# Kernel tuning notes

Hardware: AMD Instinct MI355X
Metric: run time of the kernel (lower is better)

The kernel has to match this reference:

```python
import jax, jax.numpy as jnp
import numpy as np

ANCHORS = np.array([[30.0, 61.0], [62.0, 45.0], [59.0, 119.0]], dtype=np.float32)
STRIDE = 16.0
NUM_CLASSES = 80
NB, NH, NW, NT = 16, 64, 64, 50
IGNORE_THRESH = 0.5


def _iou_cxcywh(b1, b2):
    # b1, b2: broadcastable (..., 4) boxes in (cx, cy, w, h); faithful to multi_bbox_ious(x1y1x2y2=False)
    x1, y1, w1, h1 = b1[..., 0], b1[..., 1], b1[..., 2], b1[..., 3]
    x2, y2, w2, h2 = b2[..., 0], b2[..., 1], b2[..., 2], b2[..., 3]
    mx = jnp.minimum(x1 - w1 * 0.5, x2 - w2 * 0.5)
    Mx = jnp.maximum(x1 + w1 * 0.5, x2 + w2 * 0.5)
    my = jnp.minimum(y1 - h1 * 0.5, y2 - h2 * 0.5)
    My = jnp.maximum(y1 + h1 * 0.5, y2 + h2 * 0.5)
    cw = w1 + w2 - (Mx - mx)
    ch = h1 + h2 - (My - my)
    carea = jnp.where((cw <= 0) | (ch <= 0), 0.0, cw * ch)
    uarea = w1 * h1 + w2 * h2 - carea
    return carea / uarea


def _build_targets(pred_boxes, target, anchors, nH, nW):
    nB = target.shape[0]
    nA = anchors.shape[0]
    nT = target.shape[1] // 5
    nAnchors = nA * nH * nW
    pb = pred_boxes.reshape(nB, nAnchors, 4)
    tbox = target.reshape(nB, nT, 5)
    # torch loop breaks at first target with x == 0 -> prefix validity mask
    valid = jnp.cumprod((tbox[:, :, 1] != 0).astype(jnp.int32), axis=1) > 0
    gx = tbox[:, :, 1] * nW
    gy = tbox[:, :, 2] * nH
    gw = tbox[:, :, 3] * nW
    gh = tbox[:, :, 4] * nH
    gt = jnp.stack([gx, gy, gw, gh], axis=-1)                    # (nB, nT, 4)
    ious = _iou_cxcywh(pb[:, None, :, :], gt[:, :, None, :])     # (nB, nT, nAnchors)
    cur_ious = jnp.max(jnp.where(valid[:, :, None], ious, 0.0), axis=1)
    conf_mask = jnp.where(cur_ious > IGNORE_THRESH, 0.0, 1.0).reshape(nB, nA, nH, nW)
    # best anchor per gt: IoU between zero-centered gt and zero-centered anchors
    anc0 = jnp.concatenate([jnp.zeros_like(anchors), anchors], axis=1)      # (nA, 4)
    gt0 = jnp.concatenate([jnp.zeros_like(gt[..., :2]), gt[..., 2:]], -1)   # (nB, nT, 4)
    a_ious = _iou_cxcywh(gt0[:, :, None, :], anc0[None, None, :, :])        # (nB, nT, nA)
    best_n = jnp.argmax(a_ious, axis=2)  # first-max, matches torch.max tie-break
    gi = jnp.clip(jnp.floor(gx).astype(jnp.int32), 0, nW - 1)
    gj = jnp.clip(jnp.floor(gy).astype(jnp.int32), 0, nH - 1)
    tx = gx - gi.astype(gx.dtype)
    ty = gy - gj.astype(gy.dtype)
    tw = jnp.log(gw / anchors[best_n, 0])
    th = jnp.log(gh / anchors[best_n, 1])
    tc = tbox[:, :, 0]
    coord_mask = jnp.zeros((nB, nA, nH, nW), jnp.float32)
    cls_mask = jnp.zeros((nB, nA, nH, nW), jnp.float32)
    tconf = jnp.zeros((nB, nA, nH, nW), jnp.float32)
    tcls = jnp.zeros((nB, nA, nH, nW), jnp.float32)
    tcoord = jnp.zeros((4, nB, nA, nH, nW), jnp.float32)
    bidx = jnp.arange(nB)

    def step(carry, xs):
        coord_mask, conf_mask, cls_mask, tcoord, tconf, tcls = carry
        bn, gj_t, gi_t, v, txv, tyv, twv, thv, tcv = xs  # each (nB,)

        def upd(arr, val):
            cur = arr[bidx, bn, gj_t, gi_t]
            return arr.at[bidx, bn, gj_t, gi_t].set(jnp.where(v, val, cur))

        coord_mask = upd(coord_mask, 1.0)
        cls_mask = upd(cls_mask, 1.0)
        conf_mask = upd(conf_mask, 1.0)
        tconf = upd(tconf, 1.0)
        tcls = upd(tcls, tcv)
        vals = jnp.stack([txv, tyv, twv, thv])            # (4, nB)
        cur = tcoord[:, bidx, bn, gj_t, gi_t]
        tcoord = tcoord.at[:, bidx, bn, gj_t, gi_t].set(jnp.where(v[None, :], vals, cur))
        return (coord_mask, conf_mask, cls_mask, tcoord, tconf, tcls), None

    xs = tuple(a.T for a in (best_n, gj, gi, valid, tx, ty, tw, th, tc))  # scan over targets, sequential overwrite order as in torch
    (coord_mask, conf_mask, cls_mask, tcoord, tconf, tcls), _ = jax.lax.scan(
        step, (coord_mask, conf_mask, cls_mask, tcoord, tconf, tcls), xs)
    return coord_mask, conf_mask, cls_mask, tcoord, tconf, tcls


def _yolo_loss(output, target):
    anchors = jnp.asarray(ANCHORS / STRIDE)
    nB, nA, nC = output.shape[0], ANCHORS.shape[0], NUM_CLASSES
    nH, nW = output.shape[2], output.shape[3]
    cad = nB * nA * nH * nW
    out5 = output.reshape(nB, nA, 5 + nC, nH, nW)
    coord_raw = jnp.transpose(out5[:, :, 0:4], (2, 0, 1, 3, 4)).reshape(4, cad)
    coord = jnp.concatenate([jax.nn.sigmoid(coord_raw[0:2]), coord_raw[2:4]], axis=0)
    conf = jax.nn.sigmoid(out5[:, :, 4])                         # (nB, nA, nH, nW)
    grid_x = jnp.broadcast_to(jnp.arange(nW, dtype=jnp.float32), (nB * nA, nH, nW)).reshape(-1)
    grid_y = jnp.broadcast_to(jnp.arange(nH, dtype=jnp.float32)[:, None], (nB * nA, nH, nW)).reshape(-1)
    # NOTE: anchor-major flattening replicated faithfully from the torch source (repeat(1, nB*nH*nW))
    anchor_w = jnp.broadcast_to(anchors[:, 0:1], (nA, nB * nH * nW)).reshape(-1)
    anchor_h = jnp.broadcast_to(anchors[:, 1:2], (nA, nB * nH * nW)).reshape(-1)
    pred_boxes = jnp.stack([coord[0] + grid_x, coord[1] + grid_y,
                            jnp.exp(coord[2]) * anchor_w, jnp.exp(coord[3]) * anchor_h], axis=1)
    tgt = jax.lax.stop_gradient(target)  # torch: target.detach()
    masks = _build_targets(jax.lax.stop_gradient(pred_boxes), tgt, anchors, nH, nW)
    coord_mask, conf_mask, cls_mask, tcoord, tconf, tcls = jax.tree_util.tree_map(jax.lax.stop_gradient, masks)
    cm = coord_mask.reshape(cad)
    tcoord_f = tcoord.reshape(4, cad)
    loss_coord = 0.5 * jnp.sum((coord * cm - tcoord_f * cm) ** 2)
    loss_conf = jnp.sum((conf * conf_mask - tconf * conf_mask) ** 2)
    cls = jnp.transpose(out5[:, :, 5:], (0, 1, 3, 4, 2)).reshape(cad, nC)
    logp = jax.nn.log_softmax(cls, axis=-1)
    tcls_i = tcls.reshape(cad).astype(jnp.int32)
    picked = jnp.take_along_axis(logp, tcls_i[:, None], axis=1)[:, 0]
    loss_cls = -jnp.sum(cls_mask.reshape(cad) * picked)
    return loss_coord + loss_conf + loss_cls


def setup_inputs() -> dict:
    key = jax.random.key(0)
    k_out, kc, kx, ky, kw, kh = jax.random.split(key, 6)
    output = jax.random.normal(k_out, (NB, 3 * (5 + NUM_CLASSES), NH, NW), dtype=jnp.float32)
    cls_id = jnp.floor(jax.random.uniform(kc, (NB, NT)) * NUM_CLASSES)
    cx = jax.random.uniform(kx, (NB, NT), minval=0.02, maxval=0.98)
    cy = jax.random.uniform(ky, (NB, NT), minval=0.02, maxval=0.98)
    bw = jax.random.uniform(kw, (NB, NT), minval=0.05, maxval=0.5)
    bh = jax.random.uniform(kh, (NB, NT), minval=0.05, maxval=0.5)
    target = jnp.stack([cls_id, cx, cy, bw, bh], axis=-1).reshape(NB, NT * 5).astype(jnp.float32)
    return {"output": output, "target": target}


def reference(output, target):
    return _yolo_loss(output, target)
```

## Files before the change

kernel.cpp:

```cpp
#include <hip/hip_runtime.h>
#include <math.h>

#define NBATCH 16
#define NANCH  3
#define NHH    64
#define NWW    64
#define NTT    50
#define NCLS   80
#define HW     (NHH*NWW)
#define CELLS  (NBATCH*NANCH*HW)
#define CELLBLOCKS (CELLS/256)
#define TPB    13
#define TBLOCKS (NBATCH*TPB)
#define NPART  (TBLOCKS + CELLBLOCKS)

#define AW0 1.875f
#define AW1 3.875f
#define AW2 3.6875f
#define AH0 3.8125f
#define AH1 2.8125f
#define AH2 7.4375f

__device__ __forceinline__ void prep_targets(const float* __restrict__ target, int b, int tid,
                                             float* s_gx, float* s_gy, float* s_gw, float* s_gh,
                                             float4* s_box, float2* s_gam, int* s_meta) {
    const float* tb0 = target + b * (NTT * 5);
    float c1 = 0.f, c2 = 0.f, c3 = 0.f, c4 = 0.f;
    bool nz = false;
    if (tid < NTT) {
        c1 = tb0[tid * 5 + 1]; c2 = tb0[tid * 5 + 2];
        c3 = tb0[tid * 5 + 3]; c4 = tb0[tid * 5 + 4];
        nz = (c1 != 0.0f);
    }
    const unsigned long long mask = __ballot(nz);
    const int first_zero = __ffsll((unsigned long long)~mask) - 1;
    if (tid < NTT) {
        const bool valid = tid < first_zero;
        const float gx = c1 * NWW, gy = c2 * NHH;
        const float gw = c3 * NWW, gh = c4 * NHH;

        const float ga = gw * gh;
        const float i0 = fminf(gw, AW0) * fminf(gh, AH0);
        const float i1 = fminf(gw, AW1) * fminf(gh, AH1);
        const float i2 = fminf(gw, AW2) * fminf(gh, AH2);
        const float r0 = i0 / (ga + AW0 * AH0 - i0);
        const float r1 = i1 / (ga + AW1 * AH1 - i1);
        const float r2 = i2 / (ga + AW2 * AH2 - i2);
        int best = 0; float bv = r0;
        if (r1 > bv) { bv = r1; best = 1; }
        if (r2 > bv) { bv = r2; best = 2; }

        int gi = (int)floorf(gx); gi = gi < 0 ? 0 : (gi > NWW - 1 ? NWW - 1 : gi);
        int gj = (int)floorf(gy); gj = gj < 0 ? 0 : (gj > NHH - 1 ? NHH - 1 : gj);

        const int m = valid ? ((1 << 15) | (best << 12) | (gj << 6) | gi) : 0;
        s_gx[tid] = gx; s_gy[tid] = gy; s_gw[tid] = gw; s_gh[tid] = gh;
        s_box[tid] = make_float4(gx - gw * 0.5f, gx + gw * 0.5f,
                                 gy - gh * 0.5f, gy + gh * 0.5f);
        s_gam[tid] = make_float2(ga, __int_as_float(m));
        s_meta[tid] = m;
    }
}

__global__ __launch_bounds__(256) void yolo_loss_kernel(
    const float* __restrict__ out,
    const float* __restrict__ target,
    float* __restrict__ partials)
{
    __shared__ float  s_gx[NTT], s_gy[NTT], s_gw[NTT], s_gh[NTT];
    __shared__ float4 s_box[NTT];
    __shared__ float2 s_gam[NTT];
    __shared__ int    s_meta[NTT];
    __shared__ float  s_part[4];

    const int tid  = threadIdx.x;
    const int lane = tid & 63, wid = tid >> 6;

    if (blockIdx.x < TBLOCKS) {
        const int tb = blockIdx.x;
        const int b  = tb / TPB;
        const int t  = (tb % TPB) * 4 + wid;

        if (tid < 64)
            prep_targets(target, b, tid, s_gx, s_gy, s_gw, s_gh, s_box, s_gam, s_meta);
        __syncthreads();

        float nll = 0.0f;
        if (t < NTT) {
            const int m = s_meta[t];
            if (m != 0) {
                const int mv_lane = (lane < NTT) ? s_meta[lane] : 0;
                const unsigned long long dup = __ballot(lane > t && mv_lane == m);
                if (dup == 0ULL) {
                    const int best = (m >> 12) & 3;
                    const int hw   = m & 0xFFF;
                    const float* cb = out + ((size_t)(b * NANCH + best) * (5 + NCLS) + 5) * HW + hw;

                    const float l0 = cb[lane * HW];
                    const float l1 = (lane < NCLS - 64) ? cb[(lane + 64) * HW] : -INFINITY;

                    float mx = fmaxf(l0, l1);
                    #pragma unroll
                    for (int off = 32; off > 0; off >>= 1)
                        mx = fmaxf(mx, __shfl_xor(mx, off, 64));

                    float e = __expf(l0 - mx) + ((lane < NCLS - 64) ? __expf(l1 - mx) : 0.0f);
                    #pragma unroll
                    for (int off = 32; off > 0; off >>= 1)
                        e += __shfl_xor(e, off, 64);

                    if (lane == 0) {
                        const int tc = (int)target[b * (NTT * 5) + t * 5];
                        const float lt = cb[tc * HW];
                        nll = -(lt - mx - __logf(e));
                    }
                }
            }
        }
        if (lane == 0) s_part[wid] = nll;
        __syncthreads();
        if (tid == 0)
            partials[blockIdx.x] = s_part[0] + s_part[1] + s_part[2] + s_part[3];
        return;
    }

    const int cblk = blockIdx.x - TBLOCKS;
    const int b    = cblk / 48;

    const int cell = cblk * 256 + tid;
    const int rem  = cell % (NANCH * HW);
    const int a    = rem / HW;
    const int hw   = rem % HW;
    const int h    = hw >> 6;
    const int w    = hw & 63;

    const float* base = out + ((size_t)b * (NANCH * (5 + NCLS)) + (size_t)a * (5 + NCLS)) * HW + hw;
    const float r0 = base[0];
    const float r1 = base[HW];
    const float r2 = base[2 * HW];
    const float r3 = base[3 * HW];
    const float r4 = base[4 * HW];

    if (tid < 64)
        prep_targets(target, b, tid, s_gx, s_gy, s_gw, s_gh, s_box, s_gam, s_meta);
    __syncthreads();

    const float sx = __builtin_amdgcn_rcpf(1.0f + __expf(-r0));
    const float sy = __builtin_amdgcn_rcpf(1.0f + __expf(-r1));

    const int aidx = (3 * b + a) >> 4;
    const float aw = aidx == 0 ? AW0 : (aidx == 1 ? AW1 : AW2);
    const float ah = aidx == 0 ? AH0 : (aidx == 1 ? AH1 : AH2);

    const float px = sx + (float)w;
    const float py = sy + (float)h;
    const float pw = __expf(r2) * aw;
    const float ph = __expf(r3) * ah;
    const float parea = pw * ph;

    const float hx0 = px - pw * 0.5f, hx1 = px + pw * 0.5f;
    const float hy0 = py - ph * 0.5f, hy1 = py + ph * 0.5f;

    const int key = (1 << 15) | (a << 12) | (h << 6) | w;

    float curmax = 0.0f;
    int   tlast  = -1;
    #pragma unroll 5
    for (int t = 0; t < NTT; ++t) {
        const float4 bx  = s_box[t];
        const float2 gam = s_gam[t];
        const int    m   = __float_as_int(gam.y);
        const float cw = fminf(hx1, bx.y) - fmaxf(hx0, bx.x);
        const float ch = fminf(hy1, bx.w) - fmaxf(hy0, bx.z);
        const float carea = (cw <= 0.0f || ch <= 0.0f) ? 0.0f : cw * ch;
        const float uarea = parea + gam.x - carea;
        const float iou   = carea * __builtin_amdgcn_rcpf(uarea);
        curmax = fmaxf(curmax, (m != 0) ? iou : 0.0f);
        if (m == key) tlast = t;
    }

    const float conf = __builtin_amdgcn_rcpf(1.0f + __expf(-r4));
    float lsum;
    if (tlast >= 0) {
        const int best = (s_meta[tlast] >> 12) & 3;
        const float baw = best == 0 ? AW0 : (best == 1 ? AW1 : AW2);
        const float bah = best == 0 ? AH0 : (best == 1 ? AH1 : AH2);
        const float tx = s_gx[tlast] - (float)w;
        const float ty = s_gy[tlast] - (float)h;
        const float tw = __logf(s_gw[tlast] * __builtin_amdgcn_rcpf(baw));
        const float th = __logf(s_gh[tlast] * __builtin_amdgcn_rcpf(bah));

        const float dx = sx - tx, dy = sy - ty, dw = r2 - tw, dh = r3 - th;
        const float dc = conf - 1.0f;
        lsum = dc * dc + 0.5f * (dx * dx + dy * dy + dw * dw + dh * dh);
    } else {
        lsum = (curmax > 0.5f) ? 0.0f : conf * conf;
    }

    float v = lsum;
    #pragma unroll
    for (int off = 32; off > 0; off >>= 1) v += __shfl_down(v, off, 64);
    if (lane == 0) s_part[wid] = v;
    __syncthreads();
    if (tid == 0)
        partials[blockIdx.x] = s_part[0] + s_part[1] + s_part[2] + s_part[3];
}

__global__ __launch_bounds__(256) void yolo_reduce_kernel(
    const float* __restrict__ partials, float* __restrict__ loss)
{
    __shared__ float s_part[4];
    const int tid = threadIdx.x;
    float v = 0.0f;
    for (int i = tid; i < NPART; i += 256) v += partials[i];
    #pragma unroll
    for (int off = 32; off > 0; off >>= 1) v += __shfl_down(v, off, 64);
    const int lane = tid & 63, wid = tid >> 6;
    if (lane == 0) s_part[wid] = v;
    __syncthreads();
    if (tid == 0) loss[0] = s_part[0] + s_part[1] + s_part[2] + s_part[3];
}

extern "C" void kernel_launch(void* const* d_in, const int* in_sizes, int n_in,
                              void* d_out, int out_size, void* d_ws, size_t ws_size,
                              hipStream_t stream) {
    const float* out_t  = (const float*)d_in[0];
    const float* target = (const float*)d_in[1];
    float* loss     = (float*)d_out;
    float* partials = (float*)d_ws;

    yolo_loss_kernel<<<NPART, 256, 0, stream>>>(out_t, target, partials);
    yolo_reduce_kernel<<<1, 256, 0, stream>>>(partials, loss);
}
```

Measured before the change: 96.13 us.

## Fold class-NLL target blocks into cell blocks and drop validity check in IoU loop

Removes the separate 208 target-only blocks and has the first 13 cell blocks of each batch also compute the per-target class log-softmax NLL, so the grid is just the cell blocks. Invalid targets get an empty box (inf/-inf bounds), which lets the IoU loop drop the per-target validity select. The reduce kernel is unrolled to exactly three partial loads per thread. Some cell blocks now do extra serial work after their main loop, which can lengthen the tail.

```diff
diff --git a/kernel.cpp b/kernel.cpp
--- a/kernel.cpp
+++ b/kernel.cpp
@@ -10,9 +10,7 @@
 #define HW     (NHH*NWW)
 #define CELLS  (NBATCH*NANCH*HW)
 #define CELLBLOCKS (CELLS/256)
-#define TPB    13
-#define TBLOCKS (NBATCH*TPB)
-#define NPART  (TBLOCKS + CELLBLOCKS)
+#define NPART  CELLBLOCKS
 
 #define AW0 1.875f
 #define AW1 3.875f
@@ -54,9 +52,11 @@
         int gj = (int)floorf(gy); gj = gj < 0 ? 0 : (gj > NHH - 1 ? NHH - 1 : gj);
 
         const int m = valid ? ((1 << 15) | (best << 12) | (gj << 6) | gi) : 0;
+        const float inf = __int_as_float(0x7f800000);
         s_gx[tid] = gx; s_gy[tid] = gy; s_gw[tid] = gw; s_gh[tid] = gh;
-        s_box[tid] = make_float4(gx - gw * 0.5f, gx + gw * 0.5f,
-                                 gy - gh * 0.5f, gy + gh * 0.5f);
+        s_box[tid] = valid ? make_float4(gx - gw * 0.5f, gx + gw * 0.5f,
+                                         gy - gh * 0.5f, gy + gh * 0.5f)
+                           : make_float4(inf, -inf, inf, -inf);
         s_gam[tid] = make_float2(ga, __int_as_float(m));
         s_meta[tid] = m;
     }
@@ -76,56 +76,9 @@
     const int tid  = threadIdx.x;
     const int lane = tid & 63, wid = tid >> 6;
 
-    if (blockIdx.x < TBLOCKS) {
-        const int tb = blockIdx.x;
-        const int b  = tb / TPB;
-        const int t  = (tb % TPB) * 4 + wid;
-
-        if (tid < 64)
-            prep_targets(target, b, tid, s_gx, s_gy, s_gw, s_gh, s_box, s_gam, s_meta);
-        __syncthreads();
-
-        float nll = 0.0f;
-        if (t < NTT) {
-            const int m = s_meta[t];
-            if (m != 0) {
-                const int mv_lane = (lane < NTT) ? s_meta[lane] : 0;
-                const unsigned long long dup = __ballot(lane > t && mv_lane == m);
-                if (dup == 0ULL) {
-                    const int best = (m >> 12) & 3;
-                    const int hw   = m & 0xFFF;
-                    const float* cb = out + ((size_t)(b * NANCH + best) * (5 + NCLS) + 5) * HW + hw;
-
-                    const float l0 = cb[lane * HW];
-                    const float l1 = (lane < NCLS - 64) ? cb[(lane + 64) * HW] : -INFINITY;
-
-                    float mx = fmaxf(l0, l1);
-                    #pragma unroll
-                    for (int off = 32; off > 0; off >>= 1)
-                        mx = fmaxf(mx, __shfl_xor(mx, off, 64));
-
-                    float e = __expf(l0 - mx) + ((lane < NCLS - 64) ? __expf(l1 - mx) : 0.0f);
-                    #pragma unroll
-                    for (int off = 32; off > 0; off >>= 1)
-                        e += __shfl_xor(e, off, 64);
-
-                    if (lane == 0) {
-                        const int tc = (int)target[b * (NTT * 5) + t * 5];
-                        const float lt = cb[tc * HW];
-                        nll = -(lt - mx - __logf(e));
-                    }
-                }
-            }
-        }
-        if (lane == 0) s_part[wid] = nll;
-        __syncthreads();
-        if (tid == 0)
-            partials[blockIdx.x] = s_part[0] + s_part[1] + s_part[2] + s_part[3];
-        return;
-    }
-
-    const int cblk = blockIdx.x - TBLOCKS;
+    const int cblk = blockIdx.x;
     const int b    = cblk / 48;
+    const int sub  = cblk % 48;
 
     const int cell = cblk * 256 + tid;
     const int rem  = cell % (NANCH * HW);
@@ -134,7 +87,7 @@
     const int h    = hw >> 6;
     const int w    = hw & 63;
 
-    const float* base = out + ((size_t)b * (NANCH * (5 + NCLS)) + (size_t)a * (5 + NCLS)) * HW + hw;
+    const float* base = out + ((size_t)(b * NANCH + a) * (5 + NCLS)) * HW + hw;
     const float r0 = base[0];
     const float r1 = base[HW];
     const float r2 = base[2 * HW];
@@ -169,14 +122,12 @@
     for (int t = 0; t < NTT; ++t) {
         const float4 bx  = s_box[t];
         const float2 gam = s_gam[t];
-        const int    m   = __float_as_int(gam.y);
         const float cw = fminf(hx1, bx.y) - fmaxf(hx0, bx.x);
         const float ch = fminf(hy1, bx.w) - fmaxf(hy0, bx.z);
         const float carea = (cw <= 0.0f || ch <= 0.0f) ? 0.0f : cw * ch;
         const float uarea = parea + gam.x - carea;
-        const float iou   = carea * __builtin_amdgcn_rcpf(uarea);
-        curmax = fmaxf(curmax, (m != 0) ? iou : 0.0f);
-        if (m == key) tlast = t;
+        curmax = fmaxf(curmax, carea * __builtin_amdgcn_rcpf(uarea));
+        if (__float_as_int(gam.y) == key) tlast = t;
     }
 
     const float conf = __builtin_amdgcn_rcpf(1.0f + __expf(-r4));
@@ -197,13 +148,48 @@
         lsum = (curmax > 0.5f) ? 0.0f : conf * conf;
     }
 
+    if (sub < 13) {
+        const int t = sub * 4 + wid;
+        if (t < NTT) {
+            const int m = s_meta[t];
+            if (m != 0) {
+                const int mv_lane = (lane < NTT) ? s_meta[lane] : 0;
+                const unsigned long long dup = __ballot(lane > t && mv_lane == m);
+                if (dup == 0ULL) {
+                    const int best = (m >> 12) & 3;
+                    const int thw  = m & 0xFFF;
+                    const float* cb = out + ((size_t)(b * NANCH + best) * (5 + NCLS) + 5) * HW + thw;
+
+                    const float l0 = cb[lane * HW];
+                    const float l1 = (lane < NCLS - 64) ? cb[(lane + 64) * HW] : -INFINITY;
+
+                    float mx = fmaxf(l0, l1);
+                    #pragma unroll
+                    for (int off = 32; off > 0; off >>= 1)
+                        mx = fmaxf(mx, __shfl_xor(mx, off, 64));
+
+                    float e = __expf(l0 - mx) + ((lane < NCLS - 64) ? __expf(l1 - mx) : 0.0f);
+                    #pragma unroll
+                    for (int off = 32; off > 0; off >>= 1)
+                        e += __shfl_xor(e, off, 64);
+
+                    if (lane == 0) {
+                        const int tc = (int)target[b * (NTT * 5) + t * 5];
+                        const float lt = cb[tc * HW];
+                        lsum += -(lt - mx - __logf(e));
+                    }
+                }
+            }
+        }
+    }
+
     float v = lsum;
     #pragma unroll
     for (int off = 32; off > 0; off >>= 1) v += __shfl_down(v, off, 64);
     if (lane == 0) s_part[wid] = v;
     __syncthreads();
     if (tid == 0)
-        partials[blockIdx.x] = s_part[0] + s_part[1] + s_part[2] + s_part[3];
+        partials[cblk] = s_part[0] + s_part[1] + s_part[2] + s_part[3];
 }
 
 __global__ __launch_bounds__(256) void yolo_reduce_kernel(
@@ -211,8 +197,7 @@
 {
     __shared__ float s_part[4];
     const int tid = threadIdx.x;
-    float v = 0.0f;
-    for (int i = tid; i < NPART; i += 256) v += partials[i];
+    float v = partials[tid] + partials[tid + 256] + partials[tid + 512];
     #pragma unroll
     for (int off = 32; off > 0; off >>= 1) v += __shfl_down(v, off, 64);
     const int lane = tid & 63, wid = tid >> 6;
@@ -229,6 +214,6 @@
     float* loss     = (float*)d_out;
     float* partials = (float*)d_ws;
 
-    yolo_loss_kernel<<<NPART, 256, 0, stream>>>(out_t, target, partials);
+    yolo_loss_kernel<<<CELLBLOCKS, 256, 0, stream>>>(out_t, target, partials);
     yolo_reduce_kernel<<<1, 256, 0, stream>>>(partials, loss);
 }
```

New measurement: 94.89 us, median of 2. About the same (-1.3%).
